# Optimization experiments

Measured on AMD Instinct MI355X. Metric: run time of the kernel, lower is better.

Reference implementation:

```python
import jax, jax.numpy as jnp
import numpy as np

IMG, P, C = 512, 16, 1
D, DEPTH, H, DH, MLP = 768, 12, 8, 64, 2048
GRID = IMG // P          # 32
NP = GRID * GRID         # 1024 patches
N = NP + 1               # +cls token
EPS = 1e-5


def _ln(x, s, b):
    m = jnp.mean(x, -1, keepdims=True)
    v = jnp.mean((x - m) ** 2, -1, keepdims=True)
    return (x - m) * jax.lax.rsqrt(v + EPS) * s + b


def setup_inputs() -> dict:
    key = jax.random.key(0)
    ks = jax.random.split(key, 12)
    s = 0.02
    f32 = jnp.float32
    return {
        "x": jax.random.normal(ks[0], (4, C, IMG, IMG), f32),
        "conv_w": jax.random.normal(ks[1], (D, C, P, P), f32) * s,   # [out,in,kh,kw] like torch
        "conv_b": jnp.zeros((D,), f32),
        "cls_token": jax.random.normal(ks[2], (1, 1, D), f32),
        "pos_emb": jax.random.normal(ks[3], (1, N, D), f32),
        "qkv_w": jax.random.normal(ks[4], (DEPTH, D, 3 * H * DH), f32) * s,  # [in,out] layout
        "merge_w": jax.random.normal(ks[5], (DEPTH, H * DH, D), f32) * s,
        "merge_b": jnp.zeros((DEPTH, D), f32),
        "ln1_s": jnp.ones((DEPTH, D), f32),
        "ln1_b": jnp.zeros((DEPTH, D), f32),
        "ln2_s": jnp.ones((DEPTH, D), f32),
        "ln2_b": jnp.zeros((DEPTH, D), f32),
        "ffn_w1": jax.random.normal(ks[6], (DEPTH, D, MLP), f32) * s,
        "ffn_b1": jnp.zeros((DEPTH, MLP), f32),
        "ffn_w2": jax.random.normal(ks[7], (DEPTH, MLP, D), f32) * s,
        "ffn_b2": jnp.zeros((DEPTH, D), f32),
        "lnf_s": jnp.ones((D,), f32),
        "lnf_b": jnp.zeros((D,), f32),
    }


def reference(x, conv_w, conv_b, cls_token, pos_emb, qkv_w, merge_w, merge_b,
              ln1_s, ln1_b, ln2_s, ln2_b, ffn_w1, ffn_b1, ffn_w2, ffn_b2,
              lnf_s, lnf_b):
    B = x.shape[0]
    # Patch embed: stride-P conv == non-overlapping patch extraction + matmul
    xr = x.reshape(B, C, GRID, P, GRID, P)
    tok = jnp.einsum('bchpwq,dcpq->bhwd', xr, conv_w).reshape(B, NP, D) + conv_b
    t = jnp.concatenate([jnp.broadcast_to(cls_token, (B, 1, D)), tok], axis=1)
    t = t + pos_emb  # dropout is identity in eval
    scale = DH ** -0.5
    for i in range(DEPTH):
        # MSA with pre-LN
        h = _ln(t, ln1_s[i], ln1_b[i])
        qkv = (h @ qkv_w[i]).reshape(B, N, H, 3, DH)   # [B,N,H,3,DH]
        q = jnp.transpose(qkv[..., 0, :], (0, 2, 1, 3))  # [B,H,N,DH]
        k = jnp.transpose(qkv[..., 1, :], (0, 2, 1, 3))
        v = jnp.transpose(qkv[..., 2, :], (0, 2, 1, 3))
        att = jax.nn.softmax(jnp.einsum('bhnd,bhmd->bhnm', q, k) * scale, axis=-1)
        o = jnp.einsum('bhnm,bhmd->bhnd', att, v)
        o = jnp.transpose(o, (0, 2, 1, 3)).reshape(B, N, H * DH)
        t = t + (o @ merge_w[i] + merge_b[i])
        # FFN with pre-LN, exact (erf) GELU like torch nn.GELU
        h2 = _ln(t, ln2_s[i], ln2_b[i])
        f = jax.nn.gelu(h2 @ ffn_w1[i] + ffn_b1[i], approximate=False)
        t = t + (f @ ffn_w2[i] + ffn_b2[i])
    return _ln(t, lnf_s, lnf_b)
```

## Files before the change

kernel.cpp:

```cpp
#include <hip/hip_runtime.h>

#define DEV __device__ __forceinline__

typedef short s8v __attribute__((ext_vector_type(8)));
typedef float f4v __attribute__((ext_vector_type(4)));

DEV short f2bf(float f) {
  unsigned u = __float_as_uint(f);
  u += 0x7FFFu + ((u >> 16) & 1u);
  return (short)(u >> 16);
}
DEV float bf2f(short s) { return __uint_as_float(((unsigned)(unsigned short)s) << 16); }

DEV void gld_lds16(const short* g, short* l) {
  __builtin_amdgcn_global_load_lds(
      (const __attribute__((address_space(1))) void*)g,
      (__attribute__((address_space(3))) void*)l, 16, 0, 0);
}

DEV int xcd_swz(int id, int nwg) {
  int q8 = nwg >> 3, r8 = nwg & 7, xcd = id & 7, off = id >> 3;
  return (xcd < r8) ? (xcd * (q8 + 1) + off) : (r8 * (q8 + 1) + (xcd - r8) * q8 + off);
}

__global__ __launch_bounds__(256) void gemm64(
    const short* __restrict__ A, const short* __restrict__ B, void* __restrict__ Cv,
    const float* __restrict__ bias,
    int M, int N, int K, int lda, int ldb, int ldc, int flags)
{
  __shared__ __align__(16) short As[2][64 * 64];
  __shared__ __align__(16) short Bs[2][128 * 64];
  int nwg = gridDim.x * gridDim.y;
  int idl = blockIdx.y * gridDim.x + blockIdx.x;
  int swz = xcd_swz(idl, nwg);
  int bx = swz % gridDim.x, by = swz / gridDim.x;
  int m0 = by * 64, n0 = bx * 128;
  int tid = threadIdx.x, lane = tid & 63, w = tid >> 6;
  int lr = lane & 15, kg = lane >> 4;
  f4v acc[4][2] = {};
  int NT = K >> 6;

#define STAGE(bufi, k0)                                                   \
  {                                                                       \
    _Pragma("unroll")                                                     \
    for (int p = 0; p < 2; ++p) {                                         \
      int ch = p * 256 + w * 64 + lane;                                   \
      int row = ch >> 3, c = (ch & 7) ^ (row & 7);                        \
      gld_lds16(A + (long)(m0 + row) * lda + (k0) + c * 8,                \
                &As[bufi][(p * 256 + w * 64) * 8]);                       \
    }                                                                     \
    _Pragma("unroll")                                                     \
    for (int p = 0; p < 4; ++p) {                                         \
      int ch = p * 256 + w * 64 + lane;                                   \
      int row = ch >> 3, c = (ch & 7) ^ (row & 7);                        \
      gld_lds16(B + (long)(n0 + row) * ldb + (k0) + c * 8,                \
                &Bs[bufi][(p * 256 + w * 64) * 8]);                       \
    }                                                                     \
  }

  STAGE(0, 0)
  for (int t = 0; t < NT; ++t) {
    int buf = t & 1;
    if (t + 1 < NT) {
      STAGE(buf ^ 1, (t + 1) * 64)
      asm volatile("s_waitcnt vmcnt(6)" ::: "memory");
    } else {
      asm volatile("s_waitcnt vmcnt(0)" ::: "memory");
    }
    __builtin_amdgcn_s_barrier();
    #pragma unroll
    for (int ks = 0; ks < 2; ++ks) {
      s8v av[4], bv[2];
      #pragma unroll
      for (int mi = 0; mi < 4; ++mi) {
        int row = mi * 16 + lr;
        int sl = (ks * 4 + kg) ^ (row & 7);
        av[mi] = *(const s8v*)&As[buf][row * 64 + sl * 8];
      }
      #pragma unroll
      for (int ni = 0; ni < 2; ++ni) {
        int row = w * 32 + ni * 16 + lr;
        int sl = (ks * 4 + kg) ^ (row & 7);
        bv[ni] = *(const s8v*)&Bs[buf][row * 64 + sl * 8];
      }
      #pragma unroll
      for (int mi = 0; mi < 4; ++mi)
        #pragma unroll
        for (int ni = 0; ni < 2; ++ni)
          acc[mi][ni] = __builtin_amdgcn_mfma_f32_16x16x32_bf16(av[mi], bv[ni], acc[mi][ni], 0, 0, 0);
    }
    asm volatile("s_waitcnt lgkmcnt(0)" ::: "memory");
    __builtin_amdgcn_s_barrier();
  }
#undef STAGE

  float* Cf = (float*)Cv;
  short* Cb = (short*)Cv;
  #pragma unroll
  for (int mi = 0; mi < 4; ++mi)
    #pragma unroll
    for (int ni = 0; ni < 2; ++ni) {
      int col = n0 + w * 32 + ni * 16 + lr;
      float bvv = (flags & 1) ? bias[col] : 0.f;
      #pragma unroll
      for (int j = 0; j < 4; ++j) {
        int row = m0 + mi * 16 + kg * 4 + j;
        if (row >= M) continue;
        float v = acc[mi][ni][j] + bvv;
        if (flags & 2) v = 0.5f * v * (1.f + erff(v * 0.70710678118f));
        long ci = (long)row * ldc + col;
        if (flags & 8) Cb[ci] = f2bf(v);
        else { if (flags & 4) v += Cf[ci]; Cf[ci] = v; }
      }
    }
}

__global__ __launch_bounds__(256) void flash_k(
    const short* __restrict__ qkv, short* __restrict__ O)
{
  int swz = xcd_swz(blockIdx.x, 544);
  int z = swz / 17, qt = swz - z * 17;
  int zb = z >> 3, zh = z & 7;
  const short* base = qkv + (long)zb * 1025 * 1536 + zh * 192;
  const short* Qg = base;
  const short* Kg = base + 64;
  const short* Vg = base + 128;
  int q0 = qt * 64;
  int tid = threadIdx.x, lane = tid & 63, w = tid >> 6;
  int lr = lane & 15, kg = lane >> 4;

  __shared__ __align__(16) short Qs[64][72];
  __shared__ __align__(16) short Ks[2][64 * 64];
  __shared__ __align__(16) short Vt[2][64][72];
  __shared__ __align__(16) short Ps[4][16][72];

  for (int s = tid; s < 512; s += 256) {
    int row = s >> 3, ch = s & 7;
    s8v v = {};
    if (q0 + row < 1025) v = *(const s8v*)(Qg + (long)(q0 + row) * 1536 + ch * 8);
    *(s8v*)&Qs[row][ch * 8] = v;
  }
  __syncthreads();
  s8v aq[2];
  aq[0] = *(const s8v*)&Qs[w * 16 + lr][kg * 8];
  aq[1] = *(const s8v*)&Qs[w * 16 + lr][32 + kg * 8];

#define STAGE_K(bufi, kv0)                                                 \
  {                                                                        \
    int s0 = w * 128;                                                      \
    _Pragma("unroll")                                                      \
    for (int i = 0; i < 2; ++i) {                                          \
      int s = s0 + i * 64 + lane;                                          \
      int row = s >> 3, c = (s & 7) ^ (row & 7);                           \
      gld_lds16(Kg + (long)((kv0) + row) * 1536 + c * 8,                   \
                &Ks[bufi][(s0 + i * 64) * 8]);                             \
    }                                                                      \
  }

  f4v acc[4] = {};
  float m_run[4], l_run[4];
  #pragma unroll
  for (int j = 0; j < 4; ++j) { m_run[j] = -3.0e38f; l_run[j] = 0.f; }

  STAGE_K(0, 0)
  {
    #pragma unroll
    for (int p = 0; p < 2; ++p) {
      int s = p * 256 + tid;
      int key = s & 63, ch = s >> 6;
      s8v v = {};
      if (key < 1025) v = *(const s8v*)(Vg + (long)key * 1536 + ch * 8);
      #pragma unroll
      for (int j = 0; j < 8; ++j) Vt[0][ch * 8 + j][key] = v[j];
    }
  }
  asm volatile("s_waitcnt vmcnt(0)" ::: "memory");
  asm volatile("s_waitcnt lgkmcnt(0)" ::: "memory");
  __builtin_amdgcn_s_barrier();

  for (int kt = 0; kt < 17; ++kt) {
    int cur = kt & 1;
    int kv0 = kt * 64;
    s8v vreg[2];
    int vok[2];
    if (kt < 16) {
      STAGE_K(cur ^ 1, kv0 + 64)
      #pragma unroll
      for (int p = 0; p < 2; ++p) {
        int s = p * 256 + tid;
        int key = (s & 63) + kv0 + 64, ch = s >> 6;
        vok[p] = key < 1025;
        vreg[p] = vok[p] ? *(const s8v*)(Vg + (long)key * 1536 + ch * 8) : s8v{};
      }
    }

    f4v sa[4] = {};
    #pragma unroll
    for (int ni = 0; ni < 4; ++ni) {
      int row = ni * 16 + lr;
      #pragma unroll
      for (int ks = 0; ks < 2; ++ks) {
        int c = (ks * 4 + kg) ^ (row & 7);
        s8v bk = *(const s8v*)&Ks[cur][row * 64 + c * 8];
        sa[ni] = __builtin_amdgcn_mfma_f32_16x16x32_bf16(aq[ks], bk, sa[ni], 0, 0, 0);
      }
    }
    float sv[4][4], pv[4][4], tm[4], ts[4];
    #pragma unroll
    for (int j = 0; j < 4; ++j) tm[j] = -3.0e38f;
    #pragma unroll
    for (int ni = 0; ni < 4; ++ni) {
      bool valid = (kv0 + ni * 16 + lr) < 1025;
      #pragma unroll
      for (int j = 0; j < 4; ++j) {
        float s = valid ? sa[ni][j] * 0.125f : -3.0e38f;
        sv[ni][j] = s;
        tm[j] = fmaxf(tm[j], s);
      }
    }
    #pragma unroll
    for (int o = 1; o < 16; o <<= 1)
      #pragma unroll
      for (int j = 0; j < 4; ++j) tm[j] = fmaxf(tm[j], __shfl_xor(tm[j], o));
    float scale[4], m_new[4];
    #pragma unroll
    for (int j = 0; j < 4; ++j) {
      m_new[j] = fmaxf(m_run[j], tm[j]);
      scale[j] = __expf(m_run[j] - m_new[j]);
      m_run[j] = m_new[j];
      ts[j] = 0.f;
    }
    #pragma unroll
    for (int ni = 0; ni < 4; ++ni)
      #pragma unroll
      for (int j = 0; j < 4; ++j) {
        float p = __expf(sv[ni][j] - m_new[j]);
        pv[ni][j] = p;
        ts[j] += p;
      }
    #pragma unroll
    for (int o = 1; o < 16; o <<= 1)
      #pragma unroll
      for (int j = 0; j < 4; ++j) ts[j] += __shfl_xor(ts[j], o);
    #pragma unroll
    for (int j = 0; j < 4; ++j) l_run[j] = l_run[j] * scale[j] + ts[j];
    #pragma unroll
    for (int ni = 0; ni < 4; ++ni)
      #pragma unroll
      for (int j = 0; j < 4; ++j) acc[ni][j] *= scale[j];

    if (kt < 16) {
      #pragma unroll
      for (int p = 0; p < 2; ++p) {
        int s = p * 256 + tid;
        int key = s & 63, ch = s >> 6;
        s8v v = vok[p] ? vreg[p] : s8v{};
        #pragma unroll
        for (int j = 0; j < 8; ++j) Vt[cur ^ 1][ch * 8 + j][key] = v[j];
      }
    }

    #pragma unroll
    for (int ni = 0; ni < 4; ++ni)
      #pragma unroll
      for (int j = 0; j < 4; ++j)
        Ps[w][kg * 4 + j][ni * 16 + lr] = f2bf(pv[ni][j]);
    asm volatile("s_waitcnt lgkmcnt(0)" ::: "memory");
    s8v ap[2];
    ap[0] = *(const s8v*)&Ps[w][lr][kg * 8];
    ap[1] = *(const s8v*)&Ps[w][lr][32 + kg * 8];
    #pragma unroll
    for (int ni = 0; ni < 4; ++ni) {
      #pragma unroll
      for (int ks = 0; ks < 2; ++ks) {
        s8v bvv = *(const s8v*)&Vt[cur][ni * 16 + lr][ks * 32 + kg * 8];
        acc[ni] = __builtin_amdgcn_mfma_f32_16x16x32_bf16(ap[ks], bvv, acc[ni], 0, 0, 0);
      }
    }
    asm volatile("s_waitcnt lgkmcnt(0)" ::: "memory");
    asm volatile("s_waitcnt vmcnt(0)" ::: "memory");
    __builtin_amdgcn_s_barrier();
  }
#undef STAGE_K

  float inv[4];
  #pragma unroll
  for (int j = 0; j < 4; ++j) inv[j] = 1.f / l_run[j];
  #pragma unroll
  for (int ni = 0; ni < 4; ++ni)
    #pragma unroll
    for (int j = 0; j < 4; ++j) {
      int row = q0 + w * 16 + kg * 4 + j;
      if (row < 1025)
        O[((long)(zb * 1025 + row)) * 512 + zh * 64 + ni * 16 + lr] = f2bf(acc[ni][j] * inv[j]);
    }
}

DEV void tconv_body(const float* w, short* wt, int K, int N, int bx, int by, int tid)
{
  __shared__ float tile[32][33];
  int n0 = bx * 32, k0 = by * 32;
  int tx = tid & 31, ty = tid >> 5;
  #pragma unroll
  for (int j = 0; j < 4; ++j)
    tile[ty + j * 8][tx] = w[(long)(k0 + ty + j * 8) * N + n0 + tx];
  __syncthreads();
  #pragma unroll
  for (int j = 0; j < 4; ++j)
    wt[(long)(n0 + ty + j * 8) * K + k0 + tx] = f2bf(tile[tx][ty + j * 8]);
}

__global__ __launch_bounds__(256) void tconv4_k(
    const float* __restrict__ sq, const float* __restrict__ sm,
    const float* __restrict__ sf1, const float* __restrict__ sf2,
    short* __restrict__ dq, short* __restrict__ dm,
    short* __restrict__ df1, short* __restrict__ df2)
{
  int id = blockIdx.x, tid = threadIdx.x;
  if (id < 1152)       tconv_body(sq,  dq,  768, 1536, id % 48,          id / 48,          tid);
  else if (id < 1536)  tconv_body(sm,  dm,  512, 768,  (id - 1152) % 24, (id - 1152) / 24, tid);
  else if (id < 3072)  tconv_body(sf1, df1, 768, 2048, (id - 1536) % 64, (id - 1536) / 64, tid);
  else                 tconv_body(sf2, df2, 2048, 768, (id - 3072) % 24, (id - 3072) / 24, tid);
}

__global__ __launch_bounds__(256) void cvt_k(const float* __restrict__ in,
    short* __restrict__ out, int n)
{
  int i = blockIdx.x * 256 + threadIdx.x;
  if (i < n) out[i] = f2bf(in[i]);
}

DEV void st_ln(float* p, float v) { *p = v; }
DEV void st_ln(short* p, float v) { *p = f2bf(v); }

template<typename OT>
__global__ __launch_bounds__(256) void ln_k(const float* __restrict__ x,
    const float* __restrict__ g, const float* __restrict__ b,
    OT* __restrict__ y, int rows)
{
  int row = blockIdx.x;
  if (row >= rows) return;
  const float* xr = x + (long)row * 768;
  OT* yr = y + (long)row * 768;
  int t = threadIdx.x;
  float v0 = xr[t], v1 = xr[t + 256], v2 = xr[t + 512];
  float s = v0 + v1 + v2, s2 = v0 * v0 + v1 * v1 + v2 * v2;
  #pragma unroll
  for (int o = 32; o > 0; o >>= 1) { s += __shfl_down(s, o); s2 += __shfl_down(s2, o); }
  __shared__ float as_[4], as2_[4];
  if ((t & 63) == 0) { as_[t >> 6] = s; as2_[t >> 6] = s2; }
  __syncthreads();
  s = as_[0] + as_[1] + as_[2] + as_[3];
  s2 = as2_[0] + as2_[1] + as2_[2] + as2_[3];
  float mean = s * (1.f / 768.f);
  float var = s2 * (1.f / 768.f) - mean * mean;
  float r = rsqrtf(var + 1e-5f);
  st_ln(&yr[t],       (v0 - mean) * r * g[t]       + b[t]);
  st_ln(&yr[t + 256], (v1 - mean) * r * g[t + 256] + b[t + 256]);
  st_ln(&yr[t + 512], (v2 - mean) * r * g[t + 512] + b[t + 512]);
}

__global__ __launch_bounds__(256) void im2col_k(const float* __restrict__ x,
    short* __restrict__ A)
{
  int i = blockIdx.x * 256 + threadIdx.x;
  int k = i & 255, row = i >> 8;
  int px = k & 15, py = k >> 4;
  int gx = row & 31, gy = (row >> 5) & 31, b = row >> 10;
  A[i] = f2bf(x[((long)(b * 512) + gy * 16 + py) * 512 + gx * 16 + px]);
}

__global__ __launch_bounds__(256) void assemble_k(const short* __restrict__ tok,
    const float* __restrict__ cls, const float* __restrict__ pos, float* __restrict__ t)
{
  int i = blockIdx.x * 256 + threadIdx.x;
  int d = i % 768; int rn = i / 768; int n = rn % 1025; int b = rn / 1025;
  float v = (n == 0) ? cls[d] : bf2f(tok[((long)(b * 1024 + n - 1)) * 768 + d]);
  t[i] = v + pos[n * 768 + d];
}

extern "C" void kernel_launch(void* const* d_in, const int* in_sizes, int n_in,
                              void* d_out, int out_size, void* d_ws, size_t ws_size,
                              hipStream_t stream)
{
  const float* x       = (const float*)d_in[0];
  const float* conv_w  = (const float*)d_in[1];
  const float* conv_b  = (const float*)d_in[2];
  const float* cls     = (const float*)d_in[3];
  const float* pos     = (const float*)d_in[4];
  const float* qkv_w   = (const float*)d_in[5];
  const float* merge_w = (const float*)d_in[6];
  const float* merge_b = (const float*)d_in[7];
  const float* ln1_s   = (const float*)d_in[8];
  const float* ln1_b   = (const float*)d_in[9];
  const float* ln2_s   = (const float*)d_in[10];
  const float* ln2_b   = (const float*)d_in[11];
  const float* ffn_w1  = (const float*)d_in[12];
  const float* ffn_b1  = (const float*)d_in[13];
  const float* ffn_w2  = (const float*)d_in[14];
  const float* ffn_b2  = (const float*)d_in[15];
  const float* lnf_s   = (const float*)d_in[16];
  const float* lnf_b   = (const float*)d_in[17];

  char* wsp = (char*)d_ws;
  size_t o = 0;
  auto take = [&](size_t bytes) { char* r = wsp + o; o = (o + bytes + 255) & ~(size_t)255; return r; };
  short* wq   = (short*)take(1536ul * 768 * 2);
  short* wm   = (short*)take(768ul * 512 * 2);
  short* wf1  = (short*)take(2048ul * 768 * 2);
  short* wf2  = (short*)take(768ul * 2048 * 2);
  short* wcv  = (short*)take(768ul * 256 * 2);
  float* t    = (float*)take(4100ul * 768 * 4);
  char*  hO   = take(4352ul * 768 * 2);
  short* qkv  = (short*)take(4ul * 1025 * 1536 * 2);
  char*  fV   = take(4352ul * 2048 * 2);
  take(2ul << 20);

  short* h   = (short*)hO;
  short* O   = (short*)hO;
  short* f   = (short*)fV;
  short* imc = (short*)fV;
  short* tok = (short*)(fV + 4096ul * 256 * 2);

  dim3 blk(256);

  cvt_k<<<768, blk, 0, stream>>>(conv_w, wcv, 768 * 256);
  im2col_k<<<4096, blk, 0, stream>>>(x, imc);
  gemm64<<<dim3(6, 64), blk, 0, stream>>>(imc, wcv, tok, conv_b,
      4096, 768, 256, 256, 256, 768, 1 | 8);
  assemble_k<<<12300, blk, 0, stream>>>(tok, cls, pos, t);

  for (int i = 0; i < 12; ++i) {
    tconv4_k<<<4608, blk, 0, stream>>>(
        qkv_w + (long)i * 768 * 1536, merge_w + (long)i * 512 * 768,
        ffn_w1 + (long)i * 768 * 2048, ffn_w2 + (long)i * 2048 * 768,
        wq, wm, wf1, wf2);

    ln_k<short><<<4100, blk, 0, stream>>>(t, ln1_s + i * 768, ln1_b + i * 768, h, 4100);
    gemm64<<<dim3(12, 65), blk, 0, stream>>>(h, wq, qkv, nullptr,
        4100, 1536, 768, 768, 768, 1536, 8);
    flash_k<<<544, blk, 0, stream>>>(qkv, O);
    gemm64<<<dim3(6, 65), blk, 0, stream>>>(O, wm, t, merge_b + i * 768,
        4100, 768, 512, 512, 512, 768, 1 | 4);
    ln_k<short><<<4100, blk, 0, stream>>>(t, ln2_s + i * 768, ln2_b + i * 768, h, 4100);
    gemm64<<<dim3(16, 65), blk, 0, stream>>>(h, wf1, f, ffn_b1 + i * 2048,
        4100, 2048, 768, 768, 768, 2048, 1 | 2 | 8);
    gemm64<<<dim3(6, 65), blk, 0, stream>>>(f, wf2, t, ffn_b2 + i * 768,
        4100, 768, 2048, 2048, 2048, 768, 1 | 4);
  }
  ln_k<float><<<4100, blk, 0, stream>>>(t, lnf_s, lnf_b, (float*)d_out, 4100);
}
```

Measured before the change: 2.452 ms.

## Split flash attention over KV halves and add 64x64 GEMM tile variant

Attention is split into two KV-range halves (split-K flash), doubling the block count from 544 to 1088. Each half writes fp32 partial outputs and running max/sum, and a new combine kernel merges them into the bf16 output. Separately, the GEMM is templated on N-tile width, and the N=768 GEMMs (patch embed, merge, FFN2) use 64x64 tiles to double their grid for better CU occupancy on the 256-CU part. The cost is extra fp32 partial-buffer traffic, one more launch per layer, and less reuse per tile in the smaller GEMMs.

Result: faster. 2.320 ms (-5.4%).

```diff
diff --git a/kernel.cpp b/kernel.cpp
--- a/kernel.cpp
+++ b/kernel.cpp
@@ -23,21 +23,26 @@
   return (xcd < r8) ? (xcd * (q8 + 1) + off) : (r8 * (q8 + 1) + (xcd - r8) * q8 + off);
 }
 
-__global__ __launch_bounds__(256) void gemm64(
+template<int BN>
+__global__ __launch_bounds__(256) void gemm_t(
     const short* __restrict__ A, const short* __restrict__ B, void* __restrict__ Cv,
     const float* __restrict__ bias,
     int M, int N, int K, int lda, int ldb, int ldc, int flags)
 {
+  constexpr int BPASS = BN / 32;
+  constexpr int MI = (BN == 128) ? 4 : 2;
   __shared__ __align__(16) short As[2][64 * 64];
-  __shared__ __align__(16) short Bs[2][128 * 64];
+  __shared__ __align__(16) short Bs[2][BN * 64];
   int nwg = gridDim.x * gridDim.y;
   int idl = blockIdx.y * gridDim.x + blockIdx.x;
   int swz = xcd_swz(idl, nwg);
   int bx = swz % gridDim.x, by = swz / gridDim.x;
-  int m0 = by * 64, n0 = bx * 128;
+  int m0 = by * 64, n0 = bx * BN;
   int tid = threadIdx.x, lane = tid & 63, w = tid >> 6;
   int lr = lane & 15, kg = lane >> 4;
-  f4v acc[4][2] = {};
+  int wrb = (BN == 128) ? 0 : (w >> 1) * 32;
+  int wcb = (BN == 128) ? w * 32 : (w & 1) * 32;
+  f4v acc[MI][2] = {};
   int NT = K >> 6;
 
 #define STAGE(bufi, k0)                                                   \
@@ -50,7 +55,7 @@
                 &As[bufi][(p * 256 + w * 64) * 8]);                       \
     }                                                                     \
     _Pragma("unroll")                                                     \
-    for (int p = 0; p < 4; ++p) {                                         \
+    for (int p = 0; p < BPASS; ++p) {                                     \
       int ch = p * 256 + w * 64 + lane;                                   \
       int row = ch >> 3, c = (ch & 7) ^ (row & 7);                        \
       gld_lds16(B + (long)(n0 + row) * ldb + (k0) + c * 8,                \
@@ -63,28 +68,31 @@
     int buf = t & 1;
     if (t + 1 < NT) {
       STAGE(buf ^ 1, (t + 1) * 64)
-      asm volatile("s_waitcnt vmcnt(6)" ::: "memory");
+      if constexpr (BN == 128)
+        asm volatile("s_waitcnt vmcnt(6)" ::: "memory");
+      else
+        asm volatile("s_waitcnt vmcnt(4)" ::: "memory");
     } else {
       asm volatile("s_waitcnt vmcnt(0)" ::: "memory");
     }
     __builtin_amdgcn_s_barrier();
     #pragma unroll
     for (int ks = 0; ks < 2; ++ks) {
-      s8v av[4], bv[2];
-      #pragma unroll
-      for (int mi = 0; mi < 4; ++mi) {
-        int row = mi * 16 + lr;
+      s8v av[MI], bv[2];
+      #pragma unroll
+      for (int mi = 0; mi < MI; ++mi) {
+        int row = wrb + mi * 16 + lr;
         int sl = (ks * 4 + kg) ^ (row & 7);
         av[mi] = *(const s8v*)&As[buf][row * 64 + sl * 8];
       }
       #pragma unroll
       for (int ni = 0; ni < 2; ++ni) {
-        int row = w * 32 + ni * 16 + lr;
+        int row = wcb + ni * 16 + lr;
         int sl = (ks * 4 + kg) ^ (row & 7);
         bv[ni] = *(const s8v*)&Bs[buf][row * 64 + sl * 8];
       }
       #pragma unroll
-      for (int mi = 0; mi < 4; ++mi)
+      for (int mi = 0; mi < MI; ++mi)
         #pragma unroll
         for (int ni = 0; ni < 2; ++ni)
           acc[mi][ni] = __builtin_amdgcn_mfma_f32_16x16x32_bf16(av[mi], bv[ni], acc[mi][ni], 0, 0, 0);
@@ -97,14 +105,14 @@
   float* Cf = (float*)Cv;
   short* Cb = (short*)Cv;
   #pragma unroll
-  for (int mi = 0; mi < 4; ++mi)
+  for (int mi = 0; mi < MI; ++mi)
     #pragma unroll
     for (int ni = 0; ni < 2; ++ni) {
-      int col = n0 + w * 32 + ni * 16 + lr;
+      int col = n0 + wcb + ni * 16 + lr;
       float bvv = (flags & 1) ? bias[col] : 0.f;
       #pragma unroll
       for (int j = 0; j < 4; ++j) {
-        int row = m0 + mi * 16 + kg * 4 + j;
+        int row = m0 + wrb + mi * 16 + kg * 4 + j;
         if (row >= M) continue;
         float v = acc[mi][ni][j] + bvv;
         if (flags & 2) v = 0.5f * v * (1.f + erff(v * 0.70710678118f));
@@ -116,34 +124,35 @@
 }
 
 __global__ __launch_bounds__(256) void flash_k(
-    const short* __restrict__ qkv, short* __restrict__ O)
-{
-  int swz = xcd_swz(blockIdx.x, 544);
-  int z = swz / 17, qt = swz - z * 17;
+    const short* __restrict__ qkv, float* __restrict__ Opart, float* __restrict__ ML)
+{
+  int swz = xcd_swz(blockIdx.x, 1088);
+  int h = swz / 544, rem = swz - h * 544;
+  int z = rem / 17, qt = rem - z * 17;
   int zb = z >> 3, zh = z & 7;
   const short* base = qkv + (long)zb * 1025 * 1536 + zh * 192;
   const short* Qg = base;
   const short* Kg = base + 64;
   const short* Vg = base + 128;
   int q0 = qt * 64;
+  int kt0 = h * 9, kt_end = h ? 17 : 9;
   int tid = threadIdx.x, lane = tid & 63, w = tid >> 6;
   int lr = lane & 15, kg = lane >> 4;
 
-  __shared__ __align__(16) short Qs[64][72];
+  __shared__ __align__(16) short QPs[64][72];
   __shared__ __align__(16) short Ks[2][64 * 64];
   __shared__ __align__(16) short Vt[2][64][72];
-  __shared__ __align__(16) short Ps[4][16][72];
 
   for (int s = tid; s < 512; s += 256) {
     int row = s >> 3, ch = s & 7;
     s8v v = {};
     if (q0 + row < 1025) v = *(const s8v*)(Qg + (long)(q0 + row) * 1536 + ch * 8);
-    *(s8v*)&Qs[row][ch * 8] = v;
+    *(s8v*)&QPs[row][ch * 8] = v;
   }
   __syncthreads();
   s8v aq[2];
-  aq[0] = *(const s8v*)&Qs[w * 16 + lr][kg * 8];
-  aq[1] = *(const s8v*)&Qs[w * 16 + lr][32 + kg * 8];
+  aq[0] = *(const s8v*)&QPs[w * 16 + lr][kg * 8];
+  aq[1] = *(const s8v*)&QPs[w * 16 + lr][32 + kg * 8];
 
 #define STAGE_K(bufi, kv0)                                                 \
   {                                                                        \
@@ -162,28 +171,25 @@
   #pragma unroll
   for (int j = 0; j < 4; ++j) { m_run[j] = -3.0e38f; l_run[j] = 0.f; }
 
-  STAGE_K(0, 0)
-  {
-    #pragma unroll
-    for (int p = 0; p < 2; ++p) {
-      int s = p * 256 + tid;
-      int key = s & 63, ch = s >> 6;
-      s8v v = {};
-      if (key < 1025) v = *(const s8v*)(Vg + (long)key * 1536 + ch * 8);
-      #pragma unroll
-      for (int j = 0; j < 8; ++j) Vt[0][ch * 8 + j][key] = v[j];
-    }
+  STAGE_K(0, kt0 * 64)
+  #pragma unroll
+  for (int p = 0; p < 2; ++p) {
+    int s = p * 256 + tid;
+    int key = s & 63, ch = s >> 6;
+    s8v v = *(const s8v*)(Vg + (long)(kt0 * 64 + key) * 1536 + ch * 8);
+    #pragma unroll
+    for (int j = 0; j < 8; ++j) Vt[0][ch * 8 + j][key] = v[j];
   }
   asm volatile("s_waitcnt vmcnt(0)" ::: "memory");
   asm volatile("s_waitcnt lgkmcnt(0)" ::: "memory");
   __builtin_amdgcn_s_barrier();
 
-  for (int kt = 0; kt < 17; ++kt) {
-    int cur = kt & 1;
+  for (int kt = kt0; kt < kt_end; ++kt) {
+    int cur = (kt - kt0) & 1;
     int kv0 = kt * 64;
     s8v vreg[2];
     int vok[2];
-    if (kt < 16) {
+    if (kt + 1 < kt_end) {
       STAGE_K(cur ^ 1, kv0 + 64)
       #pragma unroll
       for (int p = 0; p < 2; ++p) {
@@ -249,7 +255,7 @@
       #pragma unroll
       for (int j = 0; j < 4; ++j) acc[ni][j] *= scale[j];
 
-    if (kt < 16) {
+    if (kt + 1 < kt_end) {
       #pragma unroll
       for (int p = 0; p < 2; ++p) {
         int s = p * 256 + tid;
@@ -264,11 +270,11 @@
     for (int ni = 0; ni < 4; ++ni)
       #pragma unroll
       for (int j = 0; j < 4; ++j)
-        Ps[w][kg * 4 + j][ni * 16 + lr] = f2bf(pv[ni][j]);
+        QPs[w * 16 + kg * 4 + j][ni * 16 + lr] = f2bf(pv[ni][j]);
     asm volatile("s_waitcnt lgkmcnt(0)" ::: "memory");
     s8v ap[2];
-    ap[0] = *(const s8v*)&Ps[w][lr][kg * 8];
-    ap[1] = *(const s8v*)&Ps[w][lr][32 + kg * 8];
+    ap[0] = *(const s8v*)&QPs[w * 16 + lr][kg * 8];
+    ap[1] = *(const s8v*)&QPs[w * 16 + lr][32 + kg * 8];
     #pragma unroll
     for (int ni = 0; ni < 4; ++ni) {
       #pragma unroll
@@ -283,17 +289,38 @@
   }
 #undef STAGE_K
 
-  float inv[4];
-  #pragma unroll
-  for (int j = 0; j < 4; ++j) inv[j] = 1.f / l_run[j];
   #pragma unroll
   for (int ni = 0; ni < 4; ++ni)
     #pragma unroll
     for (int j = 0; j < 4; ++j) {
       int row = q0 + w * 16 + kg * 4 + j;
-      if (row < 1025)
-        O[((long)(zb * 1025 + row)) * 512 + zh * 64 + ni * 16 + lr] = f2bf(acc[ni][j] * inv[j]);
-    }
+      if (row < 1025) {
+        long rbase = (long)(h * 32 + z) * 1025 + row;
+        Opart[rbase * 64 + ni * 16 + lr] = acc[ni][j];
+        if (ni == 0 && lr == 0) {
+          ML[rbase * 2]     = m_run[j];
+          ML[rbase * 2 + 1] = l_run[j];
+        }
+      }
+    }
+}
+
+__global__ __launch_bounds__(256) void fcomb_k(
+    const float* __restrict__ Opart, const float* __restrict__ ML, short* __restrict__ O)
+{
+  int idx = blockIdx.x * 256 + threadIdx.x;
+  if (idx >= 32 * 1025 * 64) return;
+  int d = idx & 63;
+  int r = idx >> 6;
+  int z = r / 1025, row = r - z * 1025;
+  float m0 = ML[(long)r * 2], l0 = ML[(long)r * 2 + 1];
+  float m1 = ML[(long)(32800 + r) * 2], l1 = ML[(long)(32800 + r) * 2 + 1];
+  float M = fmaxf(m0, m1);
+  float w0 = __expf(m0 - M), w1 = __expf(m1 - M);
+  float inv = 1.f / (l0 * w0 + l1 * w1);
+  float v = (Opart[(long)r * 64 + d] * w0 + Opart[(long)(32800 + r) * 64 + d] * w1) * inv;
+  int zb = z >> 3, zh = z & 7;
+  O[((long)(zb * 1025 + row)) * 512 + zh * 64 + d] = f2bf(v);
 }
 
 DEV void tconv_body(const float* w, short* wt, int K, int N, int bx, int by, int tid)
@@ -416,17 +443,19 @@
   char*  fV   = take(4352ul * 2048 * 2);
   take(2ul << 20);
 
-  short* h   = (short*)hO;
-  short* O   = (short*)hO;
-  short* f   = (short*)fV;
-  short* imc = (short*)fV;
-  short* tok = (short*)(fV + 4096ul * 256 * 2);
+  short* h     = (short*)hO;
+  short* O     = (short*)hO;
+  short* f     = (short*)fV;
+  short* imc   = (short*)fV;
+  short* tok   = (short*)(fV + 4096ul * 256 * 2);
+  float* Opart = (float*)fV;
+  float* ML    = (float*)(fV + 16793600);
 
   dim3 blk(256);
 
   cvt_k<<<768, blk, 0, stream>>>(conv_w, wcv, 768 * 256);
   im2col_k<<<4096, blk, 0, stream>>>(x, imc);
-  gemm64<<<dim3(6, 64), blk, 0, stream>>>(imc, wcv, tok, conv_b,
+  gemm_t<64><<<dim3(12, 64), blk, 0, stream>>>(imc, wcv, tok, conv_b,
       4096, 768, 256, 256, 256, 768, 1 | 8);
   assemble_k<<<12300, blk, 0, stream>>>(tok, cls, pos, t);
 
@@ -437,15 +466,16 @@
         wq, wm, wf1, wf2);
 
     ln_k<short><<<4100, blk, 0, stream>>>(t, ln1_s + i * 768, ln1_b + i * 768, h, 4100);
-    gemm64<<<dim3(12, 65), blk, 0, stream>>>(h, wq, qkv, nullptr,
+    gemm_t<128><<<dim3(12, 65), blk, 0, stream>>>(h, wq, qkv, nullptr,
         4100, 1536, 768, 768, 768, 1536, 8);
-    flash_k<<<544, blk, 0, stream>>>(qkv, O);
-    gemm64<<<dim3(6, 65), blk, 0, stream>>>(O, wm, t, merge_b + i * 768,
+    flash_k<<<1088, blk, 0, stream>>>(qkv, Opart, ML);
+    fcomb_k<<<8200, blk, 0, stream>>>(Opart, ML, O);
+    gemm_t<64><<<dim3(12, 65), blk, 0, stream>>>(O, wm, t, merge_b + i * 768,
         4100, 768, 512, 512, 512, 768, 1 | 4);
     ln_k<short><<<4100, blk, 0, stream>>>(t, ln2_s + i * 768, ln2_b + i * 768, h, 4100);
-    gemm64<<<dim3(16, 65), blk, 0, stream>>>(h, wf1, f, ffn_b1 + i * 2048,
+    gemm_t<128><<<dim3(16, 65), blk, 0, stream>>>(h, wf1, f, ffn_b1 + i * 2048,
         4100, 2048, 768, 768, 768, 2048, 1 | 2 | 8);
-    gemm64<<<dim3(6, 65), blk, 0, stream>>>(f, wf2, t, ffn_b2 + i * 768,
+    gemm_t<64><<<dim3(12, 65), blk, 0, stream>>>(f, wf2, t, ffn_b2 + i * 768,
         4100, 768, 2048, 2048, 2048, 768, 1 | 4);
   }
   ln_k<float><<<4100, blk, 0, stream>>>(t, lnf_s, lnf_b, (float*)d_out, 4100);
```
